# Kernel tuning notes

Measured on AMD Instinct MI355X. Metric: run time of the kernel, lower is better.

The kernel has to match this reference:

```python
import jax, jax.numpy as jnp
import numpy as np

DATA_DIM, AUG_DIM, HIDDEN, BATCH = 448, 64, 512, 1024
RTOL = ATOL = 1e-3
MAX_STEPS = 20
SAFETY, MIN_FAC, MAX_FAC = 0.9, 0.2, 10.0

# Dormand-Prince (dopri5) tableau
_A = [
    [1/5],
    [3/40, 9/40],
    [44/45, -56/15, 32/9],
    [19372/6561, -25360/2187, 64448/6561, -212/729],
    [9017/3168, -355/33, 46732/5247, 49/176, -5103/18656],
]
_B5 = [35/384, 0.0, 500/1113, 125/192, -2187/6784, 11/84]          # 5th order weights (b7 = 0, FSAL)
_E = [71/57600, 0.0, -71/16695, 71/1920, -17253/339200, 22/525, -1/40]  # b5 - b4 (error)


def setup_inputs() -> dict:
    key = jax.random.key(0)
    ks = jax.random.split(key, 7)
    s = DATA_DIM + AUG_DIM  # 512
    scale = lambda fan: 0.5 / np.sqrt(fan)
    return {
        "x": jax.random.normal(ks[0], (BATCH, DATA_DIM), dtype=jnp.float32),
        "W1": jax.random.normal(ks[1], (s, HIDDEN), dtype=jnp.float32) * scale(s),
        "b1": jax.random.normal(ks[2], (HIDDEN,), dtype=jnp.float32) * 0.01,
        "W2": jax.random.normal(ks[3], (HIDDEN, HIDDEN), dtype=jnp.float32) * scale(HIDDEN),
        "b2": jax.random.normal(ks[4], (HIDDEN,), dtype=jnp.float32) * 0.01,
        "W3": jax.random.normal(ks[5], (HIDDEN, s), dtype=jnp.float32) * scale(HIDDEN),
        "b3": jax.random.normal(ks[6], (s,), dtype=jnp.float32) * 0.01,
    }


def _rms(v):
    return jnp.sqrt(jnp.mean(jnp.square(v)))


def _integrate(y0, f):
    """Adaptive dopri5 from t=0 to t=1 (rtol=atol=1e-3), torchdiffeq-style."""
    one = jnp.float32(1.0)
    # --- initial step size (Hairer heuristic) ---
    f0 = f(y0)
    sc0 = ATOL + RTOL * jnp.abs(y0)
    d0, d1 = _rms(y0 / sc0), _rms(f0 / sc0)
    h0 = jnp.where(jnp.minimum(d0, d1) < 1e-5, 1e-6, 0.01 * d0 / jnp.maximum(d1, 1e-12))
    f1 = f(y0 + h0 * f0)
    d2 = _rms((f1 - f0) / sc0) / h0
    dmax = jnp.maximum(d1, d2)
    h1 = jnp.where(dmax <= 1e-15, jnp.maximum(1e-6, h0 * 1e-3), (0.01 / jnp.maximum(dmax, 1e-12)) ** 0.2)
    dt0 = jnp.minimum(jnp.minimum(100.0 * h0, h1), one).astype(jnp.float32)

    def step(carry, _):
        t, y, dt, fy, done = carry
        dt_c = jnp.minimum(dt, one - t)  # don't overshoot t=1
        k = [fy]
        for i in range(5):  # stages 2..6
            yi = y + dt_c * sum(a * kj for a, kj in zip(_A[i], k))
            k.append(f(yi))
        y5 = y + dt_c * sum(b * kj for b, kj in zip(_B5, k))
        k.append(f(y5))  # stage 7 (FSAL: equals f at accepted y5)
        err = dt_c * sum(e * kj for e, kj in zip(_E, k))
        sc = ATOL + RTOL * jnp.maximum(jnp.abs(y), jnp.abs(y5))
        err_norm = _rms(err / sc)
        accept = err_norm <= 1.0
        en = jnp.maximum(err_norm, 1e-10)
        dt_next = dt_c * jnp.clip(SAFETY * en ** (-0.2), MIN_FAC, MAX_FAC)
        done_new = done | (accept & (t + dt_c >= one - 1e-7))
        t_n = jnp.where(done, t, jnp.where(accept, t + dt_c, t))
        y_n = jnp.where(done, y, jnp.where(accept, y5, y))
        f_n = jnp.where(done, fy, jnp.where(accept, k[6], fy))
        dt_n = jnp.where(done, dt, dt_next)
        return (t_n, y_n, dt_n, f_n, done_new), None

    carry0 = (jnp.float32(0.0), y0, dt0, f0, jnp.array(False))
    (t, y, dt, fy, done), _ = jax.lax.scan(step, carry0, None, length=MAX_STEPS)
    return y


def reference(x, W1, b1, W2, b2, W3, b3):
    # augment: concat zeros of size AUG_DIM (augment_dim > 0 branch)
    y0 = jnp.concatenate([x, jnp.zeros((x.shape[0], AUG_DIM), dtype=x.dtype)], axis=1)

    def odefunc(y):  # 3-layer ReLU MLP, time-independent dynamics
        h = jax.nn.relu(y @ W1 + b1)
        h = jax.nn.relu(h @ W2 + b2)
        return h @ W3 + b3

    return _integrate(y0, odefunc)  # solution at t=1 (out[1] in the torch module)
```

## Files before the change

kernel.cpp:

```cpp
#include <hip/hip_runtime.h>
#include <stdint.h>

#define NBLK   256
#define NTHR   512
#define ROWS   4
#define S      512
#define KSZ    (1024*512)
#define NELEMF 524288.0f
#define CHB    65536
#define NCHK   24

typedef __attribute__((ext_vector_type(4))) float  f32x4;
typedef __attribute__((ext_vector_type(8))) short  short8;
typedef __attribute__((ext_vector_type(4))) short  s16x4;
typedef __attribute__((ext_vector_type(8))) __bf16 bf16x8;
union frag_u { short8 s; bf16x8 b; };

typedef const __attribute__((address_space(1))) void* gas_t;
typedef __attribute__((address_space(3))) void*       las_t;

#define CTR_OFF  0
#define RED_OFF  256
#define WB_OFF   65536
#define YALT_OFF (WB_OFF + NCHK*CHB)
#define K_OFF    (YALT_OFF + KSZ*4)

static __device__ const float C_A2[1] = {0.2f};
static __device__ const float C_A3[2] = {3.f/40.f, 9.f/40.f};
static __device__ const float C_A4[3] = {44.f/45.f, -56.f/15.f, 32.f/9.f};
static __device__ const float C_A5[4] = {19372.f/6561.f, -25360.f/2187.f, 64448.f/6561.f, -212.f/729.f};
static __device__ const float C_A6[5] = {9017.f/3168.f, -355.f/33.f, 46732.f/5247.f, 49.f/176.f, -5103.f/18656.f};
static __device__ const float C_B5[6] = {35.f/384.f, 0.f, 500.f/1113.f, 125.f/192.f, -2187.f/6784.f, 11.f/84.f};
#define E1f (71.f/57600.f)
#define E3f (-71.f/16695.f)
#define E4f (71.f/1920.f)
#define E5f (-17253.f/339200.f)
#define E6f (22.f/525.f)
#define E7f (-1.f/40.f)

#define WAITVM(n) asm volatile("s_waitcnt vmcnt(" #n ")" ::: "memory")
#define LGKM0     asm volatile("s_waitcnt lgkmcnt(0)" ::: "memory")
#define SB0       __builtin_amdgcn_sched_barrier(0)
#define BAR       __builtin_amdgcn_s_barrier()

__device__ __forceinline__ short f2bf(float f) {
  union { float f; uint32_t u; } v; v.f = f;
  uint32_t u = v.u;
  return (short)((u + 0x7fffu + ((u >> 16) & 1u)) >> 16);
}

extern "C" __global__ void node_zero(unsigned char* ws) {
  if (threadIdx.x == 0) *(unsigned*)(ws + CTR_OFF) = 0u;
}

extern "C" __global__ void __launch_bounds__(NTHR)
node_main(const float* __restrict__ x,
          const float* __restrict__ W1, const float* __restrict__ b1,
          const float* __restrict__ W2, const float* __restrict__ b2,
          const float* __restrict__ W3, const float* __restrict__ b3,
          float* __restrict__ out, unsigned char* __restrict__ wsb) {
  __shared__ short ring[2 * 32768];
  __shared__ short actS[2][ROWS][528];
  __shared__ float sred[24];

  const int tid  = threadIdx.x;
  const int wg   = blockIdx.x;
  const int r0   = wg * ROWS;
  const int lane = tid & 63;
  const int wv   = tid >> 6;
  const int m16  = lane & 15;
  const int kg   = lane >> 4;
  const int n0   = wv * 64;
  const int arowB = (m16 & 3) * 1056;
  const unsigned m7 = (unsigned)(m16 & 7);
  const unsigned bcolB = (unsigned)(n0 + m16) * 128u;

  unsigned* ctr = (unsigned*)(wsb + CTR_OFF);
  float*    red = (float*)(wsb + RED_OFF);
  char*     Wbb = (char*)(wsb + WB_OFF);
  float*    yAb = (float*)(wsb + YALT_OFF);
  float*    kb  = (float*)(wsb + K_OFF);

  const int srow = tid >> 7;
  const int scol = (tid & 127) * 4;
  const size_t soff = (size_t)(r0 + srow) * S + scol;

  float b1v[4], b2v[4], b3v[4];
  #pragma unroll
  for (int nt = 0; nt < 4; ++nt) {
    b1v[nt] = b1[n0 + nt * 16 + m16];
    b2v[nt] = b2[n0 + nt * 16 + m16];
    b3v[nt] = b3[n0 + nt * 16 + m16];
  }

  unsigned gt = NBLK;
  float* yloc = out;
  float* yAlt = yAb;
  int s1s = 0, s7s = 6;

  auto gbar = [&]() {
    __threadfence(); __syncthreads();
    if (tid == 0) {
      __hip_atomic_fetch_add(ctr, 1u, __ATOMIC_ACQ_REL, __HIP_MEMORY_SCOPE_AGENT);
      while (__hip_atomic_load(ctr, __ATOMIC_ACQUIRE, __HIP_MEMORY_SCOPE_AGENT) < gt)
        __builtin_amdgcn_s_sleep(2);
    }
    __syncthreads();
    if ((tid & 63) == 0)
      (void)__hip_atomic_load(ctr, __ATOMIC_ACQUIRE, __HIP_MEMORY_SCOPE_AGENT);
    __syncthreads();
    gt += NBLK;
  };

  auto block_sum = [&](float v) -> float {
    #pragma unroll
    for (int o = 32; o > 0; o >>= 1) v += __shfl_down(v, o, 64);
    if ((tid & 63) == 0) sred[tid >> 6] = v;
    __syncthreads();
    if (tid == 0) {
      float s = 0.f;
      for (int i = 0; i < 8; ++i) s += sred[i];
      sred[8] = s;
    }
    __syncthreads();
    float r = sred[8];
    __syncthreads();
    return r;
  };

  auto grid_sum = [&](const float* base) -> float {
    float v = (tid < NBLK) ? base[tid] : 0.f;
    return block_sum(v);
  };

  auto stage = [&](int g) {
    const char* gsrc = Wbb + (size_t)g * CHB + (size_t)wv * 8192 + (size_t)lane * 16;
    char* ldst = (char*)ring + (size_t)(g & 1) * CHB + (size_t)wv * 8192 + (size_t)lane * 16;
    #pragma unroll
    for (int r = 0; r < 8; ++r)
      __builtin_amdgcn_global_load_lds((gas_t)(uintptr_t)(gsrc + r * 1024),
                                       (las_t)(uint32_t)(uintptr_t)(ldst + r * 1024),
                                       16, 0, 0);
  };

  auto feval = [&](const float* coef, int nk, float dtc, float* kout, float* y5p) {
    f32x4 v = *(const f32x4*)(yloc + soff);
    for (int j = 0; j < nk; ++j) {
      const float cc = coef[j];
      if (cc == 0.f) continue;
      const int slot = (j == 0) ? s1s : j;
      v += (cc * dtc) * *(const f32x4*)(kb + (size_t)slot * KSZ + soff);
    }
    if (y5p) *(f32x4*)(y5p + soff) = v;
    stage(0); stage(1);
    {
      s16x4 pk;
      #pragma unroll
      for (int e = 0; e < 4; ++e) pk[e] = f2bf(v[e]);
      *(s16x4*)((char*)&actS[0][0][0] + srow * 1056 + scol * 2) = pk;
    }
    LGKM0; SB0; BAR;

    f32x4 acc[4];
    #pragma unroll
    for (int nt = 0; nt < 4; ++nt) acc[nt] = f32x4{0.f, 0.f, 0.f, 0.f};

    for (int g = 0; g < NCHK; ++g) {
      if (g < NCHK - 1) { WAITVM(8); } else { WAITVM(0); }
      SB0;
      {
        const short* sb = ring + (g & 1) * 32768;
        const char* aBuf = (const char*)&actS[(g >= 8 && g < 16) ? 1 : 0][0][0];
        const int kb2 = (g & 7) * 128;
        #pragma unroll
        for (int kt = 0; kt < 2; ++kt) {
          frag_u a; a.s = *(const short8*)(aBuf + arowB + kb2 + kt * 64 + kg * 16);
          const unsigned uu = (((unsigned)(kt * 4 + kg)) ^ m7) * 16u;
          const char* bp = (const char*)sb + bcolB + uu;
          #pragma unroll
          for (int nt = 0; nt < 4; ++nt) {
            frag_u bq; bq.s = *(const short8*)(bp + nt * 2048);
            acc[nt] = __builtin_amdgcn_mfma_f32_16x16x32_bf16(a.b, bq.b, acc[nt], 0, 0, 0);
          }
        }
      }
      LGKM0; SB0;
      if (g < NCHK - 2) stage(g + 2);
      if (g == 7 || g == 15) {
        char* aNext = (char*)&actS[(g == 7) ? 1 : 0][0][0];
        if (kg == 0) {
          #pragma unroll
          for (int nt = 0; nt < 4; ++nt) {
            const float bv = (g == 7) ? b1v[nt] : b2v[nt];
            #pragma unroll
            for (int r = 0; r < 4; ++r)
              *(short*)(aNext + r * 1056 + (n0 + nt * 16 + m16) * 2) =
                  f2bf(fmaxf(acc[nt][r] + bv, 0.f));
          }
        }
        #pragma unroll
        for (int nt = 0; nt < 4; ++nt) acc[nt] = f32x4{0.f, 0.f, 0.f, 0.f};
        LGKM0; SB0; BAR;
      }
    }
    if (kg == 0) {
      #pragma unroll
      for (int nt = 0; nt < 4; ++nt) {
        #pragma unroll
        for (int r = 0; r < 4; ++r)
          kout[(size_t)(r0 + r) * S + n0 + nt * 16 + m16] = acc[nt][r] + b3v[nt];
      }
    }
    __syncthreads();
  };

  {
    f32x4 vv;
    if (scol < 448) vv = *(const f32x4*)(x + (size_t)(r0 + srow) * 448 + scol);
    else            vv = f32x4{0.f, 0.f, 0.f, 0.f};
    *(f32x4*)(yloc + soff) = vv;
  }
  if (wg < 192) {
    float (*tr)[68] = (float (*)[68])ring;
    const int layerI = wg >> 6;
    const int sub = wg & 63;
    const float* W = (layerI == 0) ? W1 : ((layerI == 1) ? W2 : W3);
    const int tk = (sub >> 3) * 64, tn = (sub & 7) * 64;
    {
      const int lr = tid >> 3, lc = (tid & 7) * 8;
      const f32x4* src = (const f32x4*)(W + (size_t)(tk + lr) * S + tn + lc);
      f32x4 a = src[0], b = src[1];
      #pragma unroll
      for (int e = 0; e < 4; ++e) { tr[lr][lc + e] = a[e]; tr[lr][lc + 4 + e] = b[e]; }
    }
    __syncthreads();
    {
      const int n = tid & 63;
      #pragma unroll
      for (int j2 = 0; j2 < 2; ++j2) {
        const int g4 = (tid >> 6) + j2 * 8;
        s16x4 p;
        #pragma unroll
        for (int j = 0; j < 4; ++j) p[j] = f2bf(tr[g4 * 4 + j][n]);
        const int ncol = tn + n;
        const int kk = tk + g4 * 4;
        const int kc = kk >> 6;
        const unsigned u = (unsigned)((kk & 63) >> 3);
        const unsigned h = (unsigned)((kk >> 2) & 1);
        size_t byte = ((size_t)(layerI * 8 + kc) * 512 + ncol) * 128
                    + ((u ^ (unsigned)(ncol & 7)) * 16u + h * 8u);
        *(s16x4*)(Wbb + byte) = p;
      }
    }
    __syncthreads();
  }
  gbar();

  feval(nullptr, 0, 0.f, kb, nullptr);
  {
    f32x4 y = *(const f32x4*)(yloc + soff);
    f32x4 f = *(const f32x4*)(kb + soff);
    float ay = 0.f, af = 0.f;
    #pragma unroll
    for (int q = 0; q < 4; ++q) {
      float sc = 1e-3f + 1e-3f * fabsf(y[q]);
      float a = y[q] / sc, b = f[q] / sc;
      ay += a * a; af += b * b;
    }
    float p0 = block_sum(ay);
    float p1 = block_sum(af);
    if (tid == 0) { red[wg] = p0; red[NBLK + wg] = p1; }
  }
  gbar();
  float d1s, h0;
  {
    float a = grid_sum(red);
    float b = grid_sum(red + NBLK);
    float d0 = sqrtf(a / NELEMF); d1s = sqrtf(b / NELEMF);
    h0 = (fminf(d0, d1s) < 1e-5f) ? 1e-6f : 0.01f * d0 / fmaxf(d1s, 1e-12f);
  }

  {
    const float onec[1] = {1.f};
    feval(onec, 1, h0, kb + (size_t)1 * KSZ, nullptr);
  }
  {
    f32x4 y  = *(const f32x4*)(yloc + soff);
    f32x4 f0 = *(const f32x4*)(kb + soff);
    f32x4 f1 = *(const f32x4*)(kb + (size_t)1 * KSZ + soff);
    float acc2 = 0.f;
    #pragma unroll
    for (int q = 0; q < 4; ++q) {
      float sc = 1e-3f + 1e-3f * fabsf(y[q]);
      float d = (f1[q] - f0[q]) / sc;
      acc2 += d * d;
    }
    float p2 = block_sum(acc2);
    if (tid == 0) red[2 * NBLK + wg] = p2;
  }
  gbar();
  float dt;
  {
    float s = grid_sum(red + 2 * NBLK);
    float d2 = sqrtf(s / NELEMF) / h0;
    float dmax = fmaxf(d1s, d2);
    float h1 = (dmax <= 1e-15f) ? fmaxf(1e-6f, h0 * 1e-3f)
                                : powf(0.01f / fmaxf(dmax, 1e-12f), 0.2f);
    dt = fminf(fminf(100.f * h0, h1), 1.f);
  }

  float tcur = 0.f;
  int done = 0;
  for (int step = 0; step < 20; ++step) {
    const float dtc = fminf(dt, 1.f - tcur);
    feval(C_A2, 1, dtc, kb + (size_t)1 * KSZ, nullptr);
    feval(C_A3, 2, dtc, kb + (size_t)2 * KSZ, nullptr);
    feval(C_A4, 3, dtc, kb + (size_t)3 * KSZ, nullptr);
    feval(C_A5, 4, dtc, kb + (size_t)4 * KSZ, nullptr);
    feval(C_A6, 5, dtc, kb + (size_t)5 * KSZ, nullptr);
    feval(C_B5, 6, dtc, kb + (size_t)s7s * KSZ, yAlt);

    {
      f32x4 yv  = *(const f32x4*)(yloc + soff);
      f32x4 y5v = *(const f32x4*)(yAlt + soff);
      f32x4 k1v = *(const f32x4*)(kb + (size_t)s1s * KSZ + soff);
      f32x4 k3v = *(const f32x4*)(kb + (size_t)2   * KSZ + soff);
      f32x4 k4v = *(const f32x4*)(kb + (size_t)3   * KSZ + soff);
      f32x4 k5v = *(const f32x4*)(kb + (size_t)4   * KSZ + soff);
      f32x4 k6v = *(const f32x4*)(kb + (size_t)5   * KSZ + soff);
      f32x4 k7v = *(const f32x4*)(kb + (size_t)s7s * KSZ + soff);
      f32x4 e = E1f * k1v + E3f * k3v + E4f * k4v + E5f * k5v + E6f * k6v + E7f * k7v;
      float acc2 = 0.f;
      #pragma unroll
      for (int q = 0; q < 4; ++q) {
        float ee = dtc * e[q];
        float sc = 1e-3f + 1e-3f * fmaxf(fabsf(yv[q]), fabsf(y5v[q]));
        float rr = ee / sc;
        acc2 += rr * rr;
      }
      float p = block_sum(acc2);
      if (tid == 0) red[3 * NBLK + step * NBLK + wg] = p;
    }
    gbar();
    float err_norm = sqrtf(grid_sum(red + 3 * NBLK + step * NBLK) / NELEMF);

    const int accept = (err_norm <= 1.0f);
    const float en = fmaxf(err_norm, 1e-10f);
    float fac = 0.9f * powf(en, -0.2f);
    fac = fminf(fmaxf(fac, 0.2f), 10.0f);
    const float dt_next = dtc * fac;
    const int done_new = done | (accept && (tcur + dtc >= 1.f - 1e-7f));
    if (!done) {
      if (accept) {
        tcur += dtc;
        float* tp = yloc; yloc = yAlt; yAlt = tp;
        int ts = s1s; s1s = s7s; s7s = ts;
      }
      dt = dt_next;
    }
    done = done_new;
    if (done) break;
  }

  if (yloc != out) {
    *(f32x4*)(out + soff) = *(const f32x4*)(yloc + soff);
  }
}

extern "C" void kernel_launch(void* const* d_in, const int* in_sizes, int n_in,
                              void* d_out, int out_size, void* d_ws, size_t ws_size,
                              hipStream_t stream) {
  const float* x  = (const float*)d_in[0];
  const float* W1 = (const float*)d_in[1];
  const float* b1 = (const float*)d_in[2];
  const float* W2 = (const float*)d_in[3];
  const float* b2 = (const float*)d_in[4];
  const float* W3 = (const float*)d_in[5];
  const float* b3 = (const float*)d_in[6];
  unsigned char* ws = (unsigned char*)d_ws;

  hipLaunchKernelGGL(node_zero, dim3(1), dim3(64), 0, stream, ws);
  hipLaunchKernelGGL(node_main, dim3(NBLK), dim3(NTHR), 0, stream,
                     x, W1, b1, W2, b2, W3, b3, (float*)d_out, ws);
}
```

Measured before the change: 852.8 us.

## Split weight chunks in half and deepen LDS staging ring to four buffers

```diff
diff --git a/kernel.cpp b/kernel.cpp
--- a/kernel.cpp
+++ b/kernel.cpp
@@ -7,8 +7,8 @@
 #define S      512
 #define KSZ    (1024*512)
 #define NELEMF 524288.0f
-#define CHB    65536
-#define NCHK   24
+#define CHB    32768
+#define NCHK   48
 
 typedef __attribute__((ext_vector_type(4))) float  f32x4;
 typedef __attribute__((ext_vector_type(8))) short  short8;
@@ -59,7 +59,7 @@
           const float* __restrict__ W2, const float* __restrict__ b2,
           const float* __restrict__ W3, const float* __restrict__ b3,
           float* __restrict__ out, unsigned char* __restrict__ wsb) {
-  __shared__ short ring[2 * 32768];
+  __shared__ short ring[4 * 16384];
   __shared__ short actS[2][ROWS][528];
   __shared__ float sred[24];
 
@@ -70,10 +70,9 @@
   const int wv   = tid >> 6;
   const int m16  = lane & 15;
   const int kg   = lane >> 4;
-  const int n0   = wv * 64;
   const int arowB = (m16 & 3) * 1056;
   const unsigned m7 = (unsigned)(m16 & 7);
-  const unsigned bcolB = (unsigned)(n0 + m16) * 128u;
+  const unsigned bcolB = (unsigned)(wv * 32 + m16) * 128u;
 
   unsigned* ctr = (unsigned*)(wsb + CTR_OFF);
   float*    red = (float*)(wsb + RED_OFF);
@@ -85,12 +84,14 @@
   const int scol = (tid & 127) * 4;
   const size_t soff = (size_t)(r0 + srow) * S + scol;
 
+  int colj[4];
   float b1v[4], b2v[4], b3v[4];
   #pragma unroll
-  for (int nt = 0; nt < 4; ++nt) {
-    b1v[nt] = b1[n0 + nt * 16 + m16];
-    b2v[nt] = b2[n0 + nt * 16 + m16];
-    b3v[nt] = b3[n0 + nt * 16 + m16];
+  for (int j = 0; j < 4; ++j) {
+    colj[j] = (j >> 1) * 256 + wv * 32 + (j & 1) * 16 + m16;
+    b1v[j] = b1[colj[j]];
+    b2v[j] = b2[colj[j]];
+    b3v[j] = b3[colj[j]];
   }
 
   unsigned gt = NBLK;
@@ -133,11 +134,11 @@
     return block_sum(v);
   };
 
-  auto stage = [&](int g) {
-    const char* gsrc = Wbb + (size_t)g * CHB + (size_t)wv * 8192 + (size_t)lane * 16;
-    char* ldst = (char*)ring + (size_t)(g & 1) * CHB + (size_t)wv * 8192 + (size_t)lane * 16;
-    #pragma unroll
-    for (int r = 0; r < 8; ++r)
+  auto stage = [&](int c) {
+    const char* gsrc = Wbb + (size_t)c * CHB + (size_t)wv * 4096 + (size_t)lane * 16;
+    char* ldst = (char*)ring + (size_t)(c & 3) * CHB + (size_t)wv * 4096 + (size_t)lane * 16;
+    #pragma unroll
+    for (int r = 0; r < 4; ++r)
       __builtin_amdgcn_global_load_lds((gas_t)(uintptr_t)(gsrc + r * 1024),
                                        (las_t)(uint32_t)(uintptr_t)(ldst + r * 1024),
                                        16, 0, 0);
@@ -151,8 +152,10 @@
       const int slot = (j == 0) ? s1s : j;
       v += (cc * dtc) * *(const f32x4*)(kb + (size_t)slot * KSZ + soff);
     }
+    SB0;
+    stage(0); stage(1); stage(2); stage(3);
+    SB0;
     if (y5p) *(f32x4*)(y5p + soff) = v;
-    stage(0); stage(1);
     {
       s16x4 pk;
       #pragma unroll
@@ -163,52 +166,60 @@
 
     f32x4 acc[4];
     #pragma unroll
-    for (int nt = 0; nt < 4; ++nt) acc[nt] = f32x4{0.f, 0.f, 0.f, 0.f};
-
-    for (int g = 0; g < NCHK; ++g) {
-      if (g < NCHK - 1) { WAITVM(8); } else { WAITVM(0); }
-      SB0;
-      {
-        const short* sb = ring + (g & 1) * 32768;
-        const char* aBuf = (const char*)&actS[(g >= 8 && g < 16) ? 1 : 0][0][0];
-        const int kb2 = (g & 7) * 128;
-        #pragma unroll
-        for (int kt = 0; kt < 2; ++kt) {
-          frag_u a; a.s = *(const short8*)(aBuf + arowB + kb2 + kt * 64 + kg * 16);
-          const unsigned uu = (((unsigned)(kt * 4 + kg)) ^ m7) * 16u;
-          const char* bp = (const char*)sb + bcolB + uu;
-          #pragma unroll
-          for (int nt = 0; nt < 4; ++nt) {
-            frag_u bq; bq.s = *(const short8*)(bp + nt * 2048);
-            acc[nt] = __builtin_amdgcn_mfma_f32_16x16x32_bf16(a.b, bq.b, acc[nt], 0, 0, 0);
-          }
+    for (int j = 0; j < 4; ++j) acc[j] = f32x4{0.f, 0.f, 0.f, 0.f};
+
+    for (int kbI = 0; kbI < 24; ++kbI) {
+      const char* aBuf = (const char*)&actS[(kbI >= 8 && kbI < 16) ? 1 : 0][0][0];
+      const int kb2 = (kbI & 7) * 128;
+      frag_u a0; a0.s = *(const short8*)(aBuf + arowB + kb2 + kg * 16);
+      frag_u a1; a1.s = *(const short8*)(aBuf + arowB + kb2 + 64 + kg * 16);
+      const unsigned uu0 = (((unsigned)kg) ^ m7) * 16u;
+      const unsigned uu1 = (((unsigned)(4 + kg)) ^ m7) * 16u;
+      #pragma unroll
+      for (int half = 0; half < 2; ++half) {
+        const int c = 2 * kbI + half;
+        if (c < 45)      { WAITVM(12); }
+        else if (c == 45){ WAITVM(8);  }
+        else if (c == 46){ WAITVM(4);  }
+        else             { WAITVM(0);  }
+        SB0;
+        {
+          const char* bp = (const char*)(ring + (c & 3) * 16384) + bcolB;
+          frag_u b00; b00.s = *(const short8*)(bp + uu0);
+          frag_u b01; b01.s = *(const short8*)(bp + 2048 + uu0);
+          frag_u b10; b10.s = *(const short8*)(bp + uu1);
+          frag_u b11; b11.s = *(const short8*)(bp + 2048 + uu1);
+          acc[2*half+0] = __builtin_amdgcn_mfma_f32_16x16x32_bf16(a0.b, b00.b, acc[2*half+0], 0, 0, 0);
+          acc[2*half+1] = __builtin_amdgcn_mfma_f32_16x16x32_bf16(a0.b, b01.b, acc[2*half+1], 0, 0, 0);
+          acc[2*half+0] = __builtin_amdgcn_mfma_f32_16x16x32_bf16(a1.b, b10.b, acc[2*half+0], 0, 0, 0);
+          acc[2*half+1] = __builtin_amdgcn_mfma_f32_16x16x32_bf16(a1.b, b11.b, acc[2*half+1], 0, 0, 0);
         }
-      }
-      LGKM0; SB0;
-      if (g < NCHK - 2) stage(g + 2);
-      if (g == 7 || g == 15) {
-        char* aNext = (char*)&actS[(g == 7) ? 1 : 0][0][0];
+        LGKM0; SB0;
+        if (c + 4 < NCHK) stage(c + 4);
+      }
+      if (kbI == 7 || kbI == 15) {
+        char* aNext = (char*)&actS[(kbI == 7) ? 1 : 0][0][0];
         if (kg == 0) {
           #pragma unroll
-          for (int nt = 0; nt < 4; ++nt) {
-            const float bv = (g == 7) ? b1v[nt] : b2v[nt];
+          for (int j = 0; j < 4; ++j) {
+            const float bv = (kbI == 7) ? b1v[j] : b2v[j];
             #pragma unroll
             for (int r = 0; r < 4; ++r)
-              *(short*)(aNext + r * 1056 + (n0 + nt * 16 + m16) * 2) =
-                  f2bf(fmaxf(acc[nt][r] + bv, 0.f));
+              *(short*)(aNext + r * 1056 + colj[j] * 2) =
+                  f2bf(fmaxf(acc[j][r] + bv, 0.f));
           }
         }
         #pragma unroll
-        for (int nt = 0; nt < 4; ++nt) acc[nt] = f32x4{0.f, 0.f, 0.f, 0.f};
+        for (int j = 0; j < 4; ++j) acc[j] = f32x4{0.f, 0.f, 0.f, 0.f};
         LGKM0; SB0; BAR;
       }
     }
     if (kg == 0) {
       #pragma unroll
-      for (int nt = 0; nt < 4; ++nt) {
+      for (int j = 0; j < 4; ++j) {
         #pragma unroll
         for (int r = 0; r < 4; ++r)
-          kout[(size_t)(r0 + r) * S + n0 + nt * 16 + m16] = acc[nt][r] + b3v[nt];
+          kout[(size_t)(r0 + r) * S + colj[j]] = acc[j][r] + b3v[j];
       }
     }
     __syncthreads();
@@ -244,11 +255,14 @@
         for (int j = 0; j < 4; ++j) p[j] = f2bf(tr[g4 * 4 + j][n]);
         const int ncol = tn + n;
         const int kk = tk + g4 * 4;
-        const int kc = kk >> 6;
+        const int kblock = kk >> 6;
+        const int nhalf  = ncol >> 8;
+        const int nloc   = ncol & 255;
         const unsigned u = (unsigned)((kk & 63) >> 3);
         const unsigned h = (unsigned)((kk >> 2) & 1);
-        size_t byte = ((size_t)(layerI * 8 + kc) * 512 + ncol) * 128
-                    + ((u ^ (unsigned)(ncol & 7)) * 16u + h * 8u);
+        size_t byte = (size_t)((layerI * 8 + kblock) * 2 + nhalf) * CHB
+                    + (size_t)nloc * 128
+                    + ((u ^ (unsigned)(nloc & 7)) * 16u + h * 8u);
         *(s16x4*)(Wbb + byte) = p;
       }
     }
```

After: 835.7 us. 1.02x faster.
